# Kernel optimization log

Hardware: AMD Instinct MI355X
Metric: run time of the kernel (lower is better)

## Reference

```python
import jax, jax.numpy as jnp
import numpy as np

K_DT = 7
GAMMA_DT = 0.1
EPS = 1e-6
B_DIST = 3.0

def _make_kernels():
    # CDT kernel: exp(-dist/gamma), 7x7x7
    k = K_DT
    g = np.mgrid[0:k, 0:k, 0:k] - np.floor(k / 2)
    dist = np.sqrt((g ** 2).sum(axis=0))
    cdt_k = np.exp(-dist / GAMMA_DT)[None, None].astype(np.float32)  # [1,1,7,7,7]
    # 27-point Laplacian
    lap = (1.0 / 26.0) * np.array(
        [[[2, 3, 2], [3, 6, 3], [2, 3, 2]],
         [[3, 6, 3], [6, -88, 6], [3, 6, 3]],
         [[2, 3, 2], [3, 6, 3], [2, 3, 2]]], dtype=np.float64)
    lap_k = lap[None, None].astype(np.float32)  # [1,1,3,3,3]
    # Scharr_2 Sobel-type gradient filters
    h1_p = np.array([[[1, 0, -1]]], dtype=np.float64)
    h1 = np.array([[[47, 162, 47]]], dtype=np.float64)
    h1 = h1 / h1.sum()
    h2 = h1.transpose(1, 2, 0); h2_p = h1_p.transpose(1, 2, 0)
    h3 = h1.transpose(2, 0, 1); h3_p = h1_p.transpose(2, 0, 1)
    G1 = np.kron(np.kron(h2, h3), h1_p)
    G2 = np.kron(np.kron(h3, h1), h2_p)
    G3 = np.kron(np.kron(h1, h2), h3_p)
    sob_k = np.stack([G1, G2, G3], axis=0)[:, None].astype(np.float32)  # [3,1,3,3,3]
    return jnp.asarray(cdt_k), jnp.asarray(lap_k), jnp.asarray(sob_k)

CDT_K, LAP_K, SOB_K = _make_kernels()

def conv3d(x, w, pad):
    return jax.lax.conv_general_dilated(
        x, w, window_strides=(1, 1, 1), padding=[(pad, pad)] * 3,
        dimension_numbers=('NCDHW', 'OIDHW', 'NCDHW'))

def binary(x, th, gamma):
    return jax.nn.sigmoid((x - th) * gamma)

def cdt(x):
    return -GAMMA_DT * jnp.log(conv3d(x, CDT_K, 3) + EPS)

def setup_inputs() -> dict:
    key = jax.random.key(0)
    k1, k2, k3 = jax.random.split(key, 3)
    B, C, D, H, W = 2, 1, 128, 192, 192
    x_in = jax.random.uniform(k1, (B, C, D, H, W), dtype=jnp.float32)
    y_out = jax.random.normal(k2, (B, C, D, H, W), dtype=jnp.float32)
    y_tg = jax.random.randint(k3, (B, C, D, H, W), 0, 2).astype(jnp.float32)
    w_smp = jnp.ones((1,), dtype=jnp.float32)
    gamma_ace = jnp.full((1,), 0.1, dtype=jnp.float32)
    return {"x_in": x_in, "y_out": y_out, "y_tg": y_tg, "w_smp": w_smp, "gamma_ace": gamma_ace}

def reference(x_in, y_out, y_tg, w_smp, gamma_ace):
    w_mean = jnp.mean(w_smp)
    # ---- CE_Loss (BCEWithLogits, pos_weight=1, stable form) ----
    ce_pt = jnp.clip(y_out, 0, None) - y_out * y_tg + jnp.log1p(jnp.exp(-jnp.abs(y_out)))
    ce_pm = jnp.mean(ce_pt, axis=(1, 2, 3))  # matches torch mean over dims (1,2,3)
    loss_ce = jnp.mean(w_smp * ce_pm) / w_mean
    # ---- Dice_Loss ----
    y_p = jax.nn.sigmoid(y_out)
    inter = jnp.sum(y_p * y_tg, axis=(1, 2, 3))
    card = jnp.sum(y_p + y_tg, axis=(1, 2, 3))
    d_loss = 1.0 - 2.0 * inter / (card + EPS)
    loss_dice = jnp.mean(w_smp * d_loss) / w_mean
    # ---- DT_Loss ----
    y_p_inv = 1.0 - y_p
    yb = binary(y_p, 0.5, 200.0)
    yb_inv = binary(y_p_inv, 0.5, 200.0)
    y_tg_inv = 1.0 - y_tg
    z = cdt(yb); z_tg = cdt(y_tg); z_inv = cdt(yb_inv); z_tg_inv = cdt(y_tg_inv)
    dl1 = jnp.mean(y_tg * z) / jnp.mean(y_tg + EPS)
    dl2 = jnp.mean(y_p * z_tg) / jnp.mean(y_p + EPS)
    dl3 = jnp.mean(y_tg_inv * z_inv) / jnp.mean(y_tg_inv + EPS)
    dl4 = jnp.mean(y_p_inv * z_tg_inv) / jnp.mean(y_p_inv + EPS)
    dt_pt = dl1 + dl2 + dl3 + dl4
    loss_dt = jnp.mean(w_smp * dt_pt) / w_mean
    # ---- ACE_Loss ----
    y = binary(y_p, 0.5, 200.0)
    y1 = binary(conv3d(y, LAP_K, 1), 0.5, 200.0)        # edge detector
    s = conv3d(y, SOB_K, 1)                              # [B,3,D,H,W]
    y2 = jnp.sqrt(jnp.sum(s * s, axis=1, keepdims=True) + EPS)
    y3 = jax.nn.relu(B_DIST - cdt(y))
    y4 = binary((B_DIST - y3) * binary(y3, 0.0, 200.0), 0.1, 200.0)
    l1 = jnp.mean(x_in * y, axis=(1, 2, 3, 4)) / jnp.mean(y + EPS, axis=(1, 2, 3, 4))
    l2 = jnp.mean(x_in * y4, axis=(1, 2, 3, 4)) / jnp.mean(y4 + EPS, axis=(1, 2, 3, 4))
    E1 = jnp.mean(y * (x_in - l1[:, None, None, None, None]) ** 2) / jnp.mean(y + EPS)
    E2 = jnp.mean(y4 * (x_in - l2[:, None, None, None, None]) ** 2) / jnp.mean(y4 + EPS)
    S = jnp.mean(y1 * y2) / jnp.mean(y1 + EPS)
    ace_pt = E1 + E2 + gamma_ace[0] * S
    loss_ace = jnp.mean(w_smp * ace_pt) / w_mean
    # ---- weighted sum ----
    w_ce, w_dt, w_ace, w_dice = 1.0, 0.1, 0.1, 1.0
    return w_ce * loss_ce + w_dice * loss_dice + w_dt * loss_dt + w_ace * loss_ace
```

## Files before the change

### kernel.cpp

```cpp
#include <hip/hip_runtime.h>
#include <hip/hip_bf16.h>
#include <hip/hip_fp16.h>

#define TH 8
#define TW 64
#define DC 8
#define PH (TH+2)
#define PW (TW+2)
#define PN (PH*PW)

#define DIM_D 128
#define DIM_H 192
#define DIM_W 192
#define NREP 16

#define LOG2E 1.4426950408889634f
#define LN2   0.6931471805599453f

__device__ __forceinline__ float ex2(float x){ return __builtin_amdgcn_exp2f(x); }
__device__ __forceinline__ float lg2(float x){ return __builtin_amdgcn_logf(x); }
__device__ __forceinline__ float rcpf_(float x){ return __builtin_amdgcn_rcpf(x); }
__device__ __forceinline__ __half2 bch2(unsigned u){ return __builtin_bit_cast(__half2, u); }

struct PairH { __half2 u0[2], u1[2], u2[2]; float s1[2], s2[2]; };

__device__ __forceinline__ PairH calc_pair(const __half2* __restrict__ sp, int ty, int tx)
{
    const float S30 = 47.f/256.f, S31 = 162.f/256.f;
    __half2 c[3][4];
    #pragma unroll
    for (int r = 0; r < 3; ++r) {
        const __half2* row = sp + (ty+r)*PW + 2*tx;
        uint2 lo = *reinterpret_cast<const uint2*>(row);
        uint2 hi = *reinterpret_cast<const uint2*>(row + 2);
        c[r][0]=bch2(lo.x); c[r][1]=bch2(lo.y); c[r][2]=bch2(hi.x); c[r][3]=bch2(hi.y);
    }
    __half2 s[4], m[4]; float dj[4];
    #pragma unroll
    for (int j = 0; j < 4; ++j) {
        s[j] = __hadd2(c[0][j], c[2][j]);
        m[j] = c[1][j];
        dj[j] = __low2float(__hsub2(c[0][j], c[2][j]));
    }
    PairH P;
    __half2 mm02 = __hadd2(m[0], m[2]), mm13 = __hadd2(m[1], m[3]);
    P.u0[0] = m[1];                 P.u0[1] = m[2];
    P.u1[0] = __hadd2(s[1], mm02);  P.u1[1] = __hadd2(s[2], mm13);
    P.u2[0] = __hadd2(s[0], s[2]);  P.u2[1] = __hadd2(s[1], s[3]);
    float s0x=__low2float(s[0]), s1x=__low2float(s[1]), s2x=__low2float(s[2]), s3x=__low2float(s[3]);
    float m0x=__low2float(m[0]), m1x=__low2float(m[1]), m2x=__low2float(m[2]), m3x=__low2float(m[3]);
    P.s1[0] = S30*(s0x - s2x) + S31*(m0x - m2x);
    P.s1[1] = S30*(s1x - s3x) + S31*(m1x - m3x);
    P.s2[0] = S30*(dj[0] + dj[2]) + S31*dj[1];
    P.s2[1] = S30*(dj[1] + dj[3]) + S31*dj[2];
    return P;
}

__global__ __launch_bounds__(256) void lumen_main(
    const float* __restrict__ x_in, const float* __restrict__ y_out,
    const float* __restrict__ y_tg, double* __restrict__ gacc,
    float* __restrict__ dice_i, float* __restrict__ dice_c)
{
    __shared__ __half2 ring[4][PN];

    const int tid = threadIdx.x;
    const int b  = blockIdx.z >> 4;
    const int d0 = (blockIdx.z & 15) * DC;
    const int h0 = blockIdx.y * TH;
    const int w0 = blockIdx.x * TW;
    const unsigned base = (unsigned)b * (unsigned)(DIM_D*DIM_H*DIM_W);
    const unsigned PL = DIM_H*DIM_W;
    const int rep = (blockIdx.x + gridDim.x*(blockIdx.y + gridDim.y*blockIdx.z)) & (NREP-1);

    const int l1v = tid + 256, l2v = tid + 512;
    const int dy0 = tid / PW, dx0 = tid - dy0*PW;
    const int dy1 = l1v / PW, dx1 = l1v - dy1*PW;
    const int dy2 = l2v / PW, dx2 = l2v - dy2*PW;
    const bool w2  = (l2v < PN);
    const int sgh0 = h0-1+dy0, sgw0 = w0-1+dx0;
    const int sgh1 = h0-1+dy1, sgw1 = w0-1+dx1;
    const int sgh2 = h0-1+dy2, sgw2 = w0-1+dx2;
    const bool ok0 = ((unsigned)sgh0 < (unsigned)DIM_H) && ((unsigned)sgw0 < (unsigned)DIM_W);
    const bool ok1 = ((unsigned)sgh1 < (unsigned)DIM_H) && ((unsigned)sgw1 < (unsigned)DIM_W);
    const bool ok2 = w2 && ((unsigned)sgh2 < (unsigned)DIM_H) && ((unsigned)sgw2 < (unsigned)DIM_W);
    const unsigned soff0 = ok0 ? (unsigned)(sgh0*DIM_W + sgw0) : 0u;
    const unsigned soff1 = ok1 ? (unsigned)(sgh1*DIM_W + sgw1) : 0u;
    const unsigned soff2 = ok2 ? (unsigned)(sgh2*DIM_W + sgw2) : 0u;

    float ld_yo0, ld_tg0, ld_yo1, ld_tg1, ld_yo2, ld_tg2;

    auto LOADP = [&](int p){
        if ((unsigned)p < (unsigned)DIM_D) {
            const unsigned pb = base + (unsigned)p*PL;
            float a0 = y_out[pb + soff0], c0 = y_tg[pb + soff0];
            float a1_ = y_out[pb + soff1], c1 = y_tg[pb + soff1];
            float a2_ = y_out[pb + soff2], c2 = y_tg[pb + soff2];
            ld_yo0 = ok0 ? a0 : -1e30f;  ld_tg0 = ok0 ? c0 : 0.f;
            ld_yo1 = ok1 ? a1_ : -1e30f; ld_tg1 = ok1 ? c1 : 0.f;
            ld_yo2 = ok2 ? a2_ : -1e30f; ld_tg2 = ok2 ? c2 : 0.f;
        } else {
            ld_yo0 = -1e30f; ld_tg0 = 0.f; ld_yo1 = -1e30f; ld_tg1 = 0.f;
            ld_yo2 = -1e30f; ld_tg2 = 0.f;
        }
    };
    auto WRITEP = [&](int slot){
        float yb0 = rcpf_(1.f + ex2(-50.f*LOG2E*ld_yo0));
        ring[slot][tid] = __floats2half2_rn(yb0, ld_tg0);
        float yb1 = rcpf_(1.f + ex2(-50.f*LOG2E*ld_yo1));
        ring[slot][l1v] = __floats2half2_rn(yb1, ld_tg1);
        if (w2) {
            float yb2 = rcpf_(1.f + ex2(-50.f*LOG2E*ld_yo2));
            ring[slot][l2v] = __floats2half2_rn(yb2, ld_tg2);
        }
    };

    const int ty = tid >> 5, tx = tid & 31;
    const int gh = h0 + ty;
    const float2* xin2 = reinterpret_cast<const float2*>(x_in);
    const float2* yo2p = reinterpret_cast<const float2*>(y_out);
    const unsigned PL2 = PL >> 1;
    const unsigned cen2 = (base >> 1) + (unsigned)gh*(DIM_W/2) + (unsigned)(w0>>1) + (unsigned)tx;

    const float KC1 = 4.5399929762484854e-05f, KC2 = 7.2135410e-07f, KC3 = 3.0047e-08f;
    const float L0 = -88.f/26.f, L1 = 6.f/26.f, L2 = 3.f/26.f, L3 = 2.f/26.f;
    const float S30 = 47.f/256.f, S31 = 162.f/256.f;
    const float TFULL = 1.f + 6.f*KC1 + 12.f*KC2 + 8.f*KC3;
    const float Y4TH = 0.36787858f;

    LOADP(d0-1); WRITEP(3);
    LOADP(d0  ); WRITEP(0);
    LOADP(d0+1); WRITEP(1);
    LOADP(d0+2);
    float2 xc  = xin2[cen2 + (unsigned)d0*PL2];
    float2 yoc = yo2p[cen2 + (unsigned)d0*PL2];
    __syncthreads();
    PairH PA = calc_pair(ring[3], ty, tx);
    PairH PB = calc_pair(ring[0], ty, tx);

    float a_ce=0, a_tz=0, a_pzt=0, a_itzi=0, a_ipzti=0, a_ytg=0;
    float a_y1y2=0, a_y1=0;
    float2 aE1 = make_float2(0.f,0.f);
    float2 aEx = make_float2(0.f,0.f);
    float2 aExx= make_float2(0.f,0.f);
    float dI0=0, dI1=0, dC0=0, dC1=0;

    #pragma unroll 2
    for (int i = 0; i < DC; ++i) {
        const int d = d0 + i;
        WRITEP((i+2)&3);
        __syncthreads();
        LOADP(d+3);
        const int dn = min(d+1, DIM_D-1);
        float2 xn  = xin2[cen2 + (unsigned)dn*PL2];
        float2 yon = yo2p[cen2 + (unsigned)dn*PL2];

        PairH PC = calc_pair(ring[(i+1)&3], ty, tx);

        #pragma unroll
        for (int v = 0; v < 2; ++v) {
            __half2 q0 = __hadd2(PA.u0[v], PC.u0[v]);
            __half2 q1 = __hadd2(PA.u1[v], PC.u1[v]);
            __half2 q2 = __hadd2(PA.u2[v], PC.u2[v]);
            __half2 n1 = __hadd2(PB.u1[v], q0);
            __half2 n2 = __hadd2(PB.u2[v], q1);
            float m0x = __low2float(PB.u0[v]), m0y = __high2float(PB.u0[v]);
            float n1x = __low2float(n1), n1y = __high2float(n1);
            float n2x = __low2float(n2), n2y = __high2float(n2);
            float n3x = __low2float(q2), n3y = __high2float(q2);
            float acx = fmaf(KC3,n3x, fmaf(KC2,n2x, fmaf(KC1,n1x, m0x)));
            float act = fmaf(KC3,n3y, fmaf(KC2,n2y, fmaf(KC1,n1y, m0y)));
            float al  = fmaf(L3,n3x, fmaf(L2,n2x, fmaf(L1,n1x, L0*m0x)));
            float a1 = S30*(PA.s1[v] + PC.s1[v]) + S31*PB.s1[v];
            float a2 = S30*(PA.s2[v] + PC.s2[v]) + S31*PB.s2[v];
            float a3 = (S31*S31)*__low2float(__hsub2(PA.u0[v], PC.u0[v]))
                     + (S30*S31)*__low2float(__hsub2(PA.u1[v], PC.u1[v]))
                     + (S30*S30)*__low2float(__hsub2(PA.u2[v], PC.u2[v]));

            float t   = m0y;
            float ybc = m0x;
            float x   = v ? xc.y  : xc.x;
            float yo  = v ? yoc.y : yoc.x;

            float ayo = fabsf(yo);
            float e1  = ex2(-LOG2E*ayo);
            float inv = rcpf_(1.f + e1);
            float yp  = (yo >= 0.f) ? inv : (1.f - inv);
            a_ce += fmaxf(yo, 0.f) - yo*t + LN2*lg2(1.f + e1);

            if (v) { dI1 += yp*t; dC1 += yp + t; }
            else   { dI0 += yp*t; dC0 += yp + t; }

            float l2a = lg2(acx + 1e-6f);
            float z   = -0.1f*LN2*l2a;
            a_tz    += t*z;
            a_pzt   += yp      * (-0.1f*LN2)*lg2(act + 1e-6f);
            a_itzi  += (1.f-t) * (-0.1f*LN2)*lg2((TFULL - acx) + 1e-6f);
            a_ipzti += (1.f-yp)* (-0.1f*LN2)*lg2((TFULL - act) + 1e-6f);
            a_ytg   += t;

            float y2 = __builtin_amdgcn_sqrtf(a1*a1 + a2*a2 + a3*a3 + 1e-6f);
            bool e1b = (al > 0.5f);
            a_y1y2 += e1b ? y2 : 0.f;
            a_y1   += e1b ? 1.f : 0.f;

            float y4 = (acx < Y4TH) ? 1.f : 0.f;
            aE1.x  += ybc;            aE1.y  += y4;
            aEx.x   = fmaf(x,   ybc, aEx.x);   aEx.y   = fmaf(x,   y4, aEx.y);
            aExx.x  = fmaf(x*x, ybc, aExx.x);  aExx.y  = fmaf(x*x, y4, aExx.y);
        }

        PA = PB; PB = PC;
        xc = xn; yoc = yon;
    }

    float a_yp = (dC0 + dC1) - a_ytg;

    dI0 += __shfl_xor(dI0, 32);  dI1 += __shfl_xor(dI1, 32);
    dC0 += __shfl_xor(dC0, 32);  dC1 += __shfl_xor(dC1, 32);

    float v[15] = {a_ce, a_tz, a_pzt, a_itzi, a_ipzti, a_yp, a_ytg, a_y1y2, a_y1,
                   aE1.x, aEx.x, aExx.x, aE1.y, aEx.y, aExx.y};
    #pragma unroll
    for (int k = 0; k < 15; ++k) {
        #pragma unroll
        for (int s = 32; s > 0; s >>= 1) v[k] += __shfl_xor(v[k], s);
    }

    __syncthreads();
    float* sl = (float*)ring;
    if (tid < 128) sl[tid] = 0.f;
    __syncthreads();

    int wid = tid >> 6, lane = tid & 63;
    if (lane < 32) {
        atomicAdd(&sl[2*lane],       dI0);
        atomicAdd(&sl[2*lane+1],     dI1);
        atomicAdd(&sl[64 + 2*lane],  dC0);
        atomicAdd(&sl[64 + 2*lane+1],dC1);
    }
    if (lane == 0) {
        #pragma unroll
        for (int k = 0; k < 15; ++k) sl[128 + wid*16 + k] = v[k];
    }
    __syncthreads();

    if (tid < 15) {
        float s = sl[128+tid] + sl[144+tid] + sl[160+tid] + sl[176+tid];
        int gidx = (tid < 9) ? tid : (9 + (tid - 9)*2 + b);
        atomicAdd(&gacc[rep*24 + gidx], (double)s);
    }
    if (tid < 64) {
        atomicAdd(&dice_i[b*DIM_W + w0 + tid], sl[tid]);
        atomicAdd(&dice_c[b*DIM_W + w0 + tid], sl[64 + tid]);
    }
}

__global__ __launch_bounds__(256) void lumen_final(
    const double* __restrict__ gacc,
    const float* __restrict__ dice_i, const float* __restrict__ dice_c,
    const float* __restrict__ gamma_ace, float* __restrict__ out)
{
    __shared__ float red[4];
    __shared__ double gs[24];
    int tid = threadIdx.x;
    if (tid < 24) {
        double sr = 0.0;
        for (int r = 0; r < NREP; ++r) sr += gacc[r*24 + tid];
        gs[tid] = sr;
    }
    float s = 0.f;
    for (int i = tid; i < 2*DIM_W; i += 256) {
        float I = dice_i[i], C = dice_c[i];
        s += 1.f - 2.f*I/(C + 1e-6f);
    }
    #pragma unroll
    for (int sh = 32; sh > 0; sh >>= 1) s += __shfl_xor(s, sh);
    if ((tid & 63) == 0) red[tid >> 6] = s;
    __syncthreads();
    if (tid == 0) {
        double dice_sum = (double)red[0] + red[1] + red[2] + red[3];
        double loss_dice = dice_sum / (2.0*DIM_W);
        const double Nb = (double)DIM_D * DIM_H * DIM_W;
        const double Nt = 2.0 * Nb;
        const double eps = 1e-6;
        double loss_ce = gs[0]/Nt;
        double dl1 = (gs[1]/Nt) / ((gs[6]/Nt) + eps);
        double dl2 = (gs[2]/Nt) / ((gs[5]/Nt) + eps);
        double dl3 = (gs[3]/Nt) / (((Nt - gs[6])/Nt) + eps);
        double dl4 = (gs[4]/Nt) / (((Nt - gs[5])/Nt) + eps);
        double loss_dt = dl1 + dl2 + dl3 + dl4;
        double E1n = 0.0, E2n = 0.0;
        for (int bb = 0; bb < 2; ++bb) {
            double S1 = gs[9+bb],  Sx = gs[11+bb], Sxx = gs[13+bb];
            double l1 = (Sx/Nb) / ((S1/Nb) + eps);
            E1n += Sxx - 2.0*l1*Sx + l1*l1*S1;
            double Q1 = gs[15+bb], Qx = gs[17+bb], Qxx = gs[19+bb];
            double l2 = (Qx/Nb) / ((Q1/Nb) + eps);
            E2n += Qxx - 2.0*l2*Qx + l2*l2*Q1;
        }
        double E1 = (E1n/Nt) / (((gs[9]+gs[10])/Nt) + eps);
        double E2 = (E2n/Nt) / (((gs[15]+gs[16])/Nt) + eps);
        double S  = (gs[7]/Nt) / ((gs[8]/Nt) + eps);
        double loss_ace = E1 + E2 + (double)gamma_ace[0]*S;
        out[0] = (float)(loss_ce + loss_dice + 0.1*loss_dt + 0.1*loss_ace);
    }
}

extern "C" void kernel_launch(void* const* d_in, const int* in_sizes, int n_in,
                              void* d_out, int out_size, void* d_ws, size_t ws_size,
                              hipStream_t stream) {
    const float* x_in  = (const float*)d_in[0];
    const float* y_out = (const float*)d_in[1];
    const float* y_tg  = (const float*)d_in[2];
    const float* gamma = (const float*)d_in[4];
    float* out = (float*)d_out;

    double* gacc  = (double*)d_ws;
    float* dice_i = (float*)((char*)d_ws + 4096);
    float* dice_c = (float*)((char*)d_ws + 6144);

    hipMemsetAsync(d_ws, 0, 8192, stream);

    dim3 grid(DIM_W/TW, DIM_H/TH, 2*(DIM_D/DC));
    lumen_main<<<grid, 256, 0, stream>>>(x_in, y_out, y_tg, gacc, dice_i, dice_c);
    lumen_final<<<1, 256, 0, stream>>>(gacc, dice_i, dice_c, gamma, out);
}
```

Measured before the change: 75.06 us.

## Process two depth planes per barrier and prefetch two planes ahead

Restructures the depth loop so each iteration writes two new shared-memory planes and then does one barrier, halving the number of __syncthreads calls. Global loads for the next two planes are issued right after the barrier and converted to packed half2 words in registers, so the sigmoid work overlaps with computing the current planes. It also merges the two CDT log terms for the target into one log selected by whether the target is set, which assumes the target is binary. The cost is higher register pressure from holding two prefetched planes and an extra PairH, which may lower occupancy.

```diff
diff --git a/kernel.cpp b/kernel.cpp
--- a/kernel.cpp
+++ b/kernel.cpp
@@ -21,16 +21,17 @@
 __device__ __forceinline__ float lg2(float x){ return __builtin_amdgcn_logf(x); }
 __device__ __forceinline__ float rcpf_(float x){ return __builtin_amdgcn_rcpf(x); }
 __device__ __forceinline__ __half2 bch2(unsigned u){ return __builtin_bit_cast(__half2, u); }
+__device__ __forceinline__ unsigned h2u(__half2 h){ return __builtin_bit_cast(unsigned, h); }
 
 struct PairH { __half2 u0[2], u1[2], u2[2]; float s1[2], s2[2]; };
 
-__device__ __forceinline__ PairH calc_pair(const __half2* __restrict__ sp, int ty, int tx)
+__device__ __forceinline__ PairH calc_pair(const unsigned* __restrict__ spu, int ty, int tx)
 {
     const float S30 = 47.f/256.f, S31 = 162.f/256.f;
     __half2 c[3][4];
     #pragma unroll
     for (int r = 0; r < 3; ++r) {
-        const __half2* row = sp + (ty+r)*PW + 2*tx;
+        const unsigned* row = spu + (ty+r)*PW + 2*tx;
         uint2 lo = *reinterpret_cast<const uint2*>(row);
         uint2 hi = *reinterpret_cast<const uint2*>(row + 2);
         c[r][0]=bch2(lo.x); c[r][1]=bch2(lo.y); c[r][2]=bch2(hi.x); c[r][3]=bch2(hi.y);
@@ -61,7 +62,7 @@
     const float* __restrict__ y_tg, double* __restrict__ gacc,
     float* __restrict__ dice_i, float* __restrict__ dice_c)
 {
-    __shared__ __half2 ring[4][PN];
+    __shared__ unsigned ring[4][PN];
 
     const int tid = threadIdx.x;
     const int b  = blockIdx.z >> 4;
@@ -87,31 +88,24 @@
     const unsigned soff1 = ok1 ? (unsigned)(sgh1*DIM_W + sgw1) : 0u;
     const unsigned soff2 = ok2 ? (unsigned)(sgh2*DIM_W + sgw2) : 0u;
 
-    float ld_yo0, ld_tg0, ld_yo1, ld_tg1, ld_yo2, ld_tg2;
-
-    auto LOADP = [&](int p){
+    auto LOADP = [&](int p, unsigned* sd){
         if ((unsigned)p < (unsigned)DIM_D) {
             const unsigned pb = base + (unsigned)p*PL;
             float a0 = y_out[pb + soff0], c0 = y_tg[pb + soff0];
             float a1_ = y_out[pb + soff1], c1 = y_tg[pb + soff1];
             float a2_ = y_out[pb + soff2], c2 = y_tg[pb + soff2];
-            ld_yo0 = ok0 ? a0 : -1e30f;  ld_tg0 = ok0 ? c0 : 0.f;
-            ld_yo1 = ok1 ? a1_ : -1e30f; ld_tg1 = ok1 ? c1 : 0.f;
-            ld_yo2 = ok2 ? a2_ : -1e30f; ld_tg2 = ok2 ? c2 : 0.f;
-        } else {
-            ld_yo0 = -1e30f; ld_tg0 = 0.f; ld_yo1 = -1e30f; ld_tg1 = 0.f;
-            ld_yo2 = -1e30f; ld_tg2 = 0.f;
-        }
+            float yo0 = ok0 ? a0 : -1e30f, tg0 = ok0 ? c0 : 0.f;
+            float yo1 = ok1 ? a1_ : -1e30f, tg1 = ok1 ? c1 : 0.f;
+            float yo2 = ok2 ? a2_ : -1e30f, tg2 = ok2 ? c2 : 0.f;
+            sd[0] = h2u(__floats2half2_rn(rcpf_(1.f + ex2(-50.f*LOG2E*yo0)), tg0));
+            sd[1] = h2u(__floats2half2_rn(rcpf_(1.f + ex2(-50.f*LOG2E*yo1)), tg1));
+            sd[2] = h2u(__floats2half2_rn(rcpf_(1.f + ex2(-50.f*LOG2E*yo2)), tg2));
+        } else { sd[0]=0u; sd[1]=0u; sd[2]=0u; }
     };
-    auto WRITEP = [&](int slot){
-        float yb0 = rcpf_(1.f + ex2(-50.f*LOG2E*ld_yo0));
-        ring[slot][tid] = __floats2half2_rn(yb0, ld_tg0);
-        float yb1 = rcpf_(1.f + ex2(-50.f*LOG2E*ld_yo1));
-        ring[slot][l1v] = __floats2half2_rn(yb1, ld_tg1);
-        if (w2) {
-            float yb2 = rcpf_(1.f + ex2(-50.f*LOG2E*ld_yo2));
-            ring[slot][l2v] = __floats2half2_rn(yb2, ld_tg2);
-        }
+    auto WRITEP = [&](int slot, const unsigned* sd){
+        ring[slot][tid] = sd[0];
+        ring[slot][l1v] = sd[1];
+        if (w2) ring[slot][l2v] = sd[2];
     };
 
     const int ty = tid >> 5, tx = tid & 31;
@@ -127,16 +121,6 @@
     const float TFULL = 1.f + 6.f*KC1 + 12.f*KC2 + 8.f*KC3;
     const float Y4TH = 0.36787858f;
 
-    LOADP(d0-1); WRITEP(3);
-    LOADP(d0  ); WRITEP(0);
-    LOADP(d0+1); WRITEP(1);
-    LOADP(d0+2);
-    float2 xc  = xin2[cen2 + (unsigned)d0*PL2];
-    float2 yoc = yo2p[cen2 + (unsigned)d0*PL2];
-    __syncthreads();
-    PairH PA = calc_pair(ring[3], ty, tx);
-    PairH PB = calc_pair(ring[0], ty, tx);
-
     float a_ce=0, a_tz=0, a_pzt=0, a_itzi=0, a_ipzti=0, a_ytg=0;
     float a_y1y2=0, a_y1=0;
     float2 aE1 = make_float2(0.f,0.f);
@@ -144,42 +128,32 @@
     float2 aExx= make_float2(0.f,0.f);
     float dI0=0, dI1=0, dC0=0, dC1=0;
 
-    #pragma unroll 2
-    for (int i = 0; i < DC; ++i) {
-        const int d = d0 + i;
-        WRITEP((i+2)&3);
-        __syncthreads();
-        LOADP(d+3);
-        const int dn = min(d+1, DIM_D-1);
-        float2 xn  = xin2[cen2 + (unsigned)dn*PL2];
-        float2 yon = yo2p[cen2 + (unsigned)dn*PL2];
-
-        PairH PC = calc_pair(ring[(i+1)&3], ty, tx);
-
+    auto VOXEL = [&](const PairH& A, const PairH& B, const PairH& C,
+                     float2 xc2, float2 yoc2, int d){
         #pragma unroll
         for (int v = 0; v < 2; ++v) {
-            __half2 q0 = __hadd2(PA.u0[v], PC.u0[v]);
-            __half2 q1 = __hadd2(PA.u1[v], PC.u1[v]);
-            __half2 q2 = __hadd2(PA.u2[v], PC.u2[v]);
-            __half2 n1 = __hadd2(PB.u1[v], q0);
-            __half2 n2 = __hadd2(PB.u2[v], q1);
-            float m0x = __low2float(PB.u0[v]), m0y = __high2float(PB.u0[v]);
+            __half2 q0 = __hadd2(A.u0[v], C.u0[v]);
+            __half2 q1 = __hadd2(A.u1[v], C.u1[v]);
+            __half2 q2 = __hadd2(A.u2[v], C.u2[v]);
+            __half2 n1 = __hadd2(B.u1[v], q0);
+            __half2 n2 = __hadd2(B.u2[v], q1);
+            float m0x = __low2float(B.u0[v]), m0y = __high2float(B.u0[v]);
             float n1x = __low2float(n1), n1y = __high2float(n1);
             float n2x = __low2float(n2), n2y = __high2float(n2);
             float n3x = __low2float(q2), n3y = __high2float(q2);
             float acx = fmaf(KC3,n3x, fmaf(KC2,n2x, fmaf(KC1,n1x, m0x)));
             float act = fmaf(KC3,n3y, fmaf(KC2,n2y, fmaf(KC1,n1y, m0y)));
             float al  = fmaf(L3,n3x, fmaf(L2,n2x, fmaf(L1,n1x, L0*m0x)));
-            float a1 = S30*(PA.s1[v] + PC.s1[v]) + S31*PB.s1[v];
-            float a2 = S30*(PA.s2[v] + PC.s2[v]) + S31*PB.s2[v];
-            float a3 = (S31*S31)*__low2float(__hsub2(PA.u0[v], PC.u0[v]))
-                     + (S30*S31)*__low2float(__hsub2(PA.u1[v], PC.u1[v]))
-                     + (S30*S30)*__low2float(__hsub2(PA.u2[v], PC.u2[v]));
+            float a1 = S30*(A.s1[v] + C.s1[v]) + S31*B.s1[v];
+            float a2 = S30*(A.s2[v] + C.s2[v]) + S31*B.s2[v];
+            float a3 = (S31*S31)*__low2float(__hsub2(A.u0[v], C.u0[v]))
+                     + (S30*S31)*__low2float(__hsub2(A.u1[v], C.u1[v]))
+                     + (S30*S30)*__low2float(__hsub2(A.u2[v], C.u2[v]));
 
             float t   = m0y;
             float ybc = m0x;
-            float x   = v ? xc.y  : xc.x;
-            float yo  = v ? yoc.y : yoc.x;
+            float x   = v ? xc2.y  : xc2.x;
+            float yo  = v ? yoc2.y : yoc2.x;
 
             float ayo = fabsf(yo);
             float e1  = ex2(-LOG2E*ayo);
@@ -190,11 +164,12 @@
             if (v) { dI1 += yp*t; dC1 += yp + t; }
             else   { dI0 += yp*t; dC0 += yp + t; }
 
-            float l2a = lg2(acx + 1e-6f);
-            float z   = -0.1f*LN2*l2a;
-            a_tz    += t*z;
+            bool tset = (t > 0.5f);
+            float argx = tset ? acx : (TFULL - acx);
+            float lx   = (-0.1f*LN2)*lg2(argx + 1e-6f);
+            a_tz   += tset ? lx : 0.f;
+            a_itzi += tset ? 0.f : lx;
             a_pzt   += yp      * (-0.1f*LN2)*lg2(act + 1e-6f);
-            a_itzi  += (1.f-t) * (-0.1f*LN2)*lg2((TFULL - acx) + 1e-6f);
             a_ipzti += (1.f-yp)* (-0.1f*LN2)*lg2((TFULL - act) + 1e-6f);
             a_ytg   += t;
 
@@ -204,13 +179,50 @@
             a_y1   += e1b ? 1.f : 0.f;
 
             float y4 = (acx < Y4TH) ? 1.f : 0.f;
-            aE1.x  += ybc;            aE1.y  += y4;
+            aE1.x  += ybc;                     aE1.y  += y4;
             aEx.x   = fmaf(x,   ybc, aEx.x);   aEx.y   = fmaf(x,   y4, aEx.y);
             aExx.x  = fmaf(x*x, ybc, aExx.x);  aExx.y  = fmaf(x*x, y4, aExx.y);
         }
-
-        PA = PB; PB = PC;
-        xc = xn; yoc = yon;
+    };
+
+    unsigned sA[3], sB[3];
+    LOADP(d0-1, sA); WRITEP(0, sA);
+    LOADP(d0,   sA); WRITEP(1, sA);
+    LOADP(d0+1, sA); WRITEP(2, sA);
+    LOADP(d0+2, sA);
+    LOADP(d0+3, sB);
+    float2 xc  = xin2[cen2 + (unsigned)d0*PL2];
+    float2 yoc = yo2p[cen2 + (unsigned)d0*PL2];
+    float2 xn  = xin2[cen2 + (unsigned)(d0+1)*PL2];
+    float2 yon = yo2p[cen2 + (unsigned)(d0+1)*PL2];
+    __syncthreads();
+    PairH PA = calc_pair(ring[0], ty, tx);
+    PairH PB = calc_pair(ring[1], ty, tx);
+    PairH PC = calc_pair(ring[2], ty, tx);
+
+    #pragma unroll
+    for (int i = 0; i < DC; i += 2) {
+        const int d = d0 + i;
+        WRITEP((i+3)&3, sA);
+        WRITEP(i&3, sB);
+        __syncthreads();
+        if (i < DC-2) {
+            LOADP(d+4, sA);
+            LOADP(d+5, sB);
+        }
+        const int dp2 = min(d+2, DIM_D-1), dp3 = min(d+3, DIM_D-1);
+        float2 xc2  = xin2[cen2 + (unsigned)dp2*PL2];
+        float2 yoc2 = yo2p[cen2 + (unsigned)dp2*PL2];
+        float2 xn2  = xin2[cen2 + (unsigned)dp3*PL2];
+        float2 yon2 = yo2p[cen2 + (unsigned)dp3*PL2];
+
+        PairH PD = calc_pair(ring[(i+3)&3], ty, tx);
+        VOXEL(PA, PB, PC, xc, yoc, d);
+        PairH PE = calc_pair(ring[i&3], ty, tx);
+        VOXEL(PB, PC, PD, xn, yon, d+1);
+
+        PA = PC; PB = PD; PC = PE;
+        xc = xc2; yoc = yoc2; xn = xn2; yon = yon2;
     }
 
     float a_yp = (dC0 + dC1) - a_ytg;
```

Result: slower. 81.46 us (+8.5%).

## Pack Sobel terms in half2, hoist sigmoid into load, cut log count

Applied to the files above, without the earlier changes.

The Sobel gradient partial sums are computed as packed half2 operations, two pixels per instruction, replacing the per-lane float arithmetic. The sigmoid binarisation moves from the shared-memory write into the load step, so shared memory receives ready-packed words. The CDT log terms exploit the binary target: a log near 1 (where the argument is close to 1) is replaced by a linear approximation, which removes two of the four log evaluations per voxel. This trades precision, since half-precision gradients and the linearised log only hold because targets are exactly 0 or 1, for fewer transcendental and VALU operations.

```diff
diff --git a/kernel.cpp b/kernel.cpp
--- a/kernel.cpp
+++ b/kernel.cpp
@@ -21,38 +21,48 @@
 __device__ __forceinline__ float lg2(float x){ return __builtin_amdgcn_logf(x); }
 __device__ __forceinline__ float rcpf_(float x){ return __builtin_amdgcn_rcpf(x); }
 __device__ __forceinline__ __half2 bch2(unsigned u){ return __builtin_bit_cast(__half2, u); }
-
-struct PairH { __half2 u0[2], u1[2], u2[2]; float s1[2], s2[2]; };
-
-__device__ __forceinline__ PairH calc_pair(const __half2* __restrict__ sp, int ty, int tx)
+__device__ __forceinline__ unsigned h2u(__half2 h){ return __builtin_bit_cast(unsigned, h); }
+__device__ __forceinline__ __half2 pklo(__half2 a, __half2 b){
+    return __halves2half2(__low2half(a), __low2half(b));
+}
+
+struct PairH { __half2 u0[2], u1[2], u2[2]; __half2 s1p, s2p, s3p; };
+
+__device__ __forceinline__ PairH calc_pair(const unsigned* __restrict__ spu, int ty, int tx)
 {
-    const float S30 = 47.f/256.f, S31 = 162.f/256.f;
     __half2 c[3][4];
     #pragma unroll
     for (int r = 0; r < 3; ++r) {
-        const __half2* row = sp + (ty+r)*PW + 2*tx;
+        const unsigned* row = spu + (ty+r)*PW + 2*tx;
         uint2 lo = *reinterpret_cast<const uint2*>(row);
         uint2 hi = *reinterpret_cast<const uint2*>(row + 2);
         c[r][0]=bch2(lo.x); c[r][1]=bch2(lo.y); c[r][2]=bch2(hi.x); c[r][3]=bch2(hi.y);
     }
-    __half2 s[4], m[4]; float dj[4];
+    __half2 s[4], m[4], dv[4];
     #pragma unroll
     for (int j = 0; j < 4; ++j) {
-        s[j] = __hadd2(c[0][j], c[2][j]);
-        m[j] = c[1][j];
-        dj[j] = __low2float(__hsub2(c[0][j], c[2][j]));
+        s[j]  = __hadd2(c[0][j], c[2][j]);
+        m[j]  = c[1][j];
+        dv[j] = __hsub2(c[0][j], c[2][j]);
     }
     PairH P;
     __half2 mm02 = __hadd2(m[0], m[2]), mm13 = __hadd2(m[1], m[3]);
     P.u0[0] = m[1];                 P.u0[1] = m[2];
     P.u1[0] = __hadd2(s[1], mm02);  P.u1[1] = __hadd2(s[2], mm13);
     P.u2[0] = __hadd2(s[0], s[2]);  P.u2[1] = __hadd2(s[1], s[3]);
-    float s0x=__low2float(s[0]), s1x=__low2float(s[1]), s2x=__low2float(s[2]), s3x=__low2float(s[3]);
-    float m0x=__low2float(m[0]), m1x=__low2float(m[1]), m2x=__low2float(m[2]), m3x=__low2float(m[3]);
-    P.s1[0] = S30*(s0x - s2x) + S31*(m0x - m2x);
-    P.s1[1] = S30*(s1x - s3x) + S31*(m1x - m3x);
-    P.s2[0] = S30*(dj[0] + dj[2]) + S31*dj[1];
-    P.s2[1] = S30*(dj[1] + dj[3]) + S31*dj[2];
+
+    const __half2 S30h = __float2half2_rn(47.f/256.f);
+    const __half2 S31h = __float2half2_rn(162.f/256.f);
+    P.s1p = __hfma2(S30h, __hsub2(pklo(s[0],s[1]), pklo(s[2],s[3])),
+                    __hmul2(S31h, __hsub2(pklo(m[0],m[1]), pklo(m[2],m[3]))));
+    P.s2p = __hfma2(S30h, __hadd2(pklo(dv[0],dv[1]), pklo(dv[2],dv[3])),
+                    __hmul2(S31h, pklo(dv[1],dv[2])));
+    const __half2 K33 = __float2half2_rn((162.f/256.f)*(162.f/256.f));
+    const __half2 K31 = __float2half2_rn((47.f/256.f)*(162.f/256.f));
+    const __half2 K11 = __float2half2_rn((47.f/256.f)*(47.f/256.f));
+    P.s3p = __hfma2(K33, pklo(P.u0[0],P.u0[1]),
+            __hfma2(K31, pklo(P.u1[0],P.u1[1]),
+            __hmul2(K11, pklo(P.u2[0],P.u2[1]))));
     return P;
 }
 
@@ -61,7 +71,7 @@
     const float* __restrict__ y_tg, double* __restrict__ gacc,
     float* __restrict__ dice_i, float* __restrict__ dice_c)
 {
-    __shared__ __half2 ring[4][PN];
+    __shared__ unsigned ring[4][PN];
 
     const int tid = threadIdx.x;
     const int b  = blockIdx.z >> 4;
@@ -87,31 +97,25 @@
     const unsigned soff1 = ok1 ? (unsigned)(sgh1*DIM_W + sgw1) : 0u;
     const unsigned soff2 = ok2 ? (unsigned)(sgh2*DIM_W + sgw2) : 0u;
 
-    float ld_yo0, ld_tg0, ld_yo1, ld_tg1, ld_yo2, ld_tg2;
-
+    unsigned sd[3];
     auto LOADP = [&](int p){
         if ((unsigned)p < (unsigned)DIM_D) {
             const unsigned pb = base + (unsigned)p*PL;
             float a0 = y_out[pb + soff0], c0 = y_tg[pb + soff0];
             float a1_ = y_out[pb + soff1], c1 = y_tg[pb + soff1];
             float a2_ = y_out[pb + soff2], c2 = y_tg[pb + soff2];
-            ld_yo0 = ok0 ? a0 : -1e30f;  ld_tg0 = ok0 ? c0 : 0.f;
-            ld_yo1 = ok1 ? a1_ : -1e30f; ld_tg1 = ok1 ? c1 : 0.f;
-            ld_yo2 = ok2 ? a2_ : -1e30f; ld_tg2 = ok2 ? c2 : 0.f;
-        } else {
-            ld_yo0 = -1e30f; ld_tg0 = 0.f; ld_yo1 = -1e30f; ld_tg1 = 0.f;
-            ld_yo2 = -1e30f; ld_tg2 = 0.f;
-        }
+            float yo0 = ok0 ? a0 : -1e30f, tg0 = ok0 ? c0 : 0.f;
+            float yo1 = ok1 ? a1_ : -1e30f, tg1 = ok1 ? c1 : 0.f;
+            float yo2 = ok2 ? a2_ : -1e30f, tg2 = ok2 ? c2 : 0.f;
+            sd[0] = h2u(__floats2half2_rn(rcpf_(1.f + ex2(-50.f*LOG2E*yo0)), tg0));
+            sd[1] = h2u(__floats2half2_rn(rcpf_(1.f + ex2(-50.f*LOG2E*yo1)), tg1));
+            sd[2] = h2u(__floats2half2_rn(rcpf_(1.f + ex2(-50.f*LOG2E*yo2)), tg2));
+        } else { sd[0]=0u; sd[1]=0u; sd[2]=0u; }
     };
     auto WRITEP = [&](int slot){
-        float yb0 = rcpf_(1.f + ex2(-50.f*LOG2E*ld_yo0));
-        ring[slot][tid] = __floats2half2_rn(yb0, ld_tg0);
-        float yb1 = rcpf_(1.f + ex2(-50.f*LOG2E*ld_yo1));
-        ring[slot][l1v] = __floats2half2_rn(yb1, ld_tg1);
-        if (w2) {
-            float yb2 = rcpf_(1.f + ex2(-50.f*LOG2E*ld_yo2));
-            ring[slot][l2v] = __floats2half2_rn(yb2, ld_tg2);
-        }
+        ring[slot][tid] = sd[0];
+        ring[slot][l1v] = sd[1];
+        if (w2) ring[slot][l2v] = sd[2];
     };
 
     const int ty = tid >> 5, tx = tid & 31;
@@ -123,9 +127,10 @@
 
     const float KC1 = 4.5399929762484854e-05f, KC2 = 7.2135410e-07f, KC3 = 3.0047e-08f;
     const float L0 = -88.f/26.f, L1 = 6.f/26.f, L2 = 3.f/26.f, L3 = 2.f/26.f;
-    const float S30 = 47.f/256.f, S31 = 162.f/256.f;
     const float TFULL = 1.f + 6.f*KC1 + 12.f*KC2 + 8.f*KC3;
     const float Y4TH = 0.36787858f;
+    const __half2 S30h2 = __float2half2_rn(47.f/256.f);
+    const __half2 S31h2 = __float2half2_rn(162.f/256.f);
 
     LOADP(d0-1); WRITEP(3);
     LOADP(d0  ); WRITEP(0);
@@ -155,6 +160,10 @@
         float2 yon = yo2p[cen2 + (unsigned)dn*PL2];
 
         PairH PC = calc_pair(ring[(i+1)&3], ty, tx);
+
+        __half2 a1p = __hfma2(S30h2, __hadd2(PA.s1p, PC.s1p), __hmul2(S31h2, PB.s1p));
+        __half2 a2p = __hfma2(S30h2, __hadd2(PA.s2p, PC.s2p), __hmul2(S31h2, PB.s2p));
+        __half2 a3p = __hsub2(PA.s3p, PC.s3p);
 
         #pragma unroll
         for (int v = 0; v < 2; ++v) {
@@ -170,11 +179,9 @@
             float acx = fmaf(KC3,n3x, fmaf(KC2,n2x, fmaf(KC1,n1x, m0x)));
             float act = fmaf(KC3,n3y, fmaf(KC2,n2y, fmaf(KC1,n1y, m0y)));
             float al  = fmaf(L3,n3x, fmaf(L2,n2x, fmaf(L1,n1x, L0*m0x)));
-            float a1 = S30*(PA.s1[v] + PC.s1[v]) + S31*PB.s1[v];
-            float a2 = S30*(PA.s2[v] + PC.s2[v]) + S31*PB.s2[v];
-            float a3 = (S31*S31)*__low2float(__hsub2(PA.u0[v], PC.u0[v]))
-                     + (S30*S31)*__low2float(__hsub2(PA.u1[v], PC.u1[v]))
-                     + (S30*S30)*__low2float(__hsub2(PA.u2[v], PC.u2[v]));
+            float a1 = v ? __high2float(a1p) : __low2float(a1p);
+            float a2 = v ? __high2float(a2p) : __low2float(a2p);
+            float a3 = v ? __high2float(a3p) : __low2float(a3p);
 
             float t   = m0y;
             float ybc = m0x;
@@ -190,21 +197,25 @@
             if (v) { dI1 += yp*t; dC1 += yp + t; }
             else   { dI0 += yp*t; dC0 += yp + t; }
 
-            float l2a = lg2(acx + 1e-6f);
-            float z   = -0.1f*LN2*l2a;
-            a_tz    += t*z;
-            a_pzt   += yp      * (-0.1f*LN2)*lg2(act + 1e-6f);
-            a_itzi  += (1.f-t) * (-0.1f*LN2)*lg2((TFULL - acx) + 1e-6f);
-            a_ipzti += (1.f-yp)* (-0.1f*LN2)*lg2((TFULL - act) + 1e-6f);
+            bool tset = (t > 0.5f);
+            float argx = tset ? acx : (TFULL - acx);
+            float lx   = (-0.1f*LN2)*lg2(argx + 1e-6f);
+            a_tz   += tset ? lx : 0.f;
+            a_itzi += tset ? 0.f : lx;
+            float sm_arg = tset ? (TFULL - act) : act;
+            float sm_log = (-0.1f*LN2)*lg2(sm_arg + 1e-6f);
+            float lin    = -0.1f*((tset ? (act - 1.f) : (TFULL - 1.f - act)) + 1e-6f);
+            a_pzt   += yp      * (tset ? lin    : sm_log);
+            a_ipzti += (1.f-yp)* (tset ? sm_log : lin);
             a_ytg   += t;
 
-            float y2 = __builtin_amdgcn_sqrtf(a1*a1 + a2*a2 + a3*a3 + 1e-6f);
+            float y2 = __builtin_amdgcn_sqrtf(fmaf(a1,a1, fmaf(a2,a2, fmaf(a3,a3, 1e-6f))));
             bool e1b = (al > 0.5f);
             a_y1y2 += e1b ? y2 : 0.f;
             a_y1   += e1b ? 1.f : 0.f;
 
             float y4 = (acx < Y4TH) ? 1.f : 0.f;
-            aE1.x  += ybc;            aE1.y  += y4;
+            aE1.x  += ybc;                     aE1.y  += y4;
             aEx.x   = fmaf(x,   ybc, aEx.x);   aEx.y   = fmaf(x,   y4, aEx.y);
             aExx.x  = fmaf(x*x, ybc, aExx.x);  aExx.y  = fmaf(x*x, y4, aExx.y);
         }
```

Result: faster. 71.71 us (median of 2 runs) (-4.5%).
